# Kernel optimization log

Measured on AMD Instinct MI355X. Metric: run time of the kernel, lower is better.

## Reference

```python
import jax, jax.numpy as jnp
import numpy as np

N_PTS = 1 << 20          # query points
N_LEVELS = 8
BASE_RES, MAX_RES = 16, 512
GROWTH = (MAX_RES / BASE_RES) ** (1.0 / (N_LEVELS - 1))
RES = [int(np.floor(BASE_RES * GROWTH ** i)) for i in range(N_LEVELS)]
T = 1 << 19              # hash table size per level
F = 2                    # features per table entry
D = 64                   # per-level MLP width
NUM_OUT = 16
BOUND = 1.5

# 8 corner offsets of a unit cube, and NGP spatial-hash primes
OFFSETS = np.stack(np.meshgrid(*([[0, 1]] * 3), indexing='ij'), -1).reshape(8, 3)
PRIMES = np.array([1, 2654435761, 805459861], dtype=np.uint32)


def hash_interp(xn, table, res):
    """Trilinear hash-grid lookup. xn: [N,3] in [0,1), table: [T,F]."""
    pos = xn * res                                    # [N,3]
    p0f = jnp.floor(pos)
    w = pos - jax.lax.stop_gradient(p0f)              # [N,3] interp weights
    p0 = jax.lax.stop_gradient(p0f).astype(jnp.uint32)
    corners = p0[:, None, :] + jnp.asarray(OFFSETS.astype(np.uint32))[None]  # [N,8,3]
    hp = corners * jnp.asarray(PRIMES)[None, None, :]  # uint32 wraparound mul
    idx = (hp[..., 0] ^ hp[..., 1] ^ hp[..., 2]) & jnp.uint32(T - 1)  # [N,8]
    feats = table[idx]                                # [N,8,F] irregular gather
    off = jnp.asarray(OFFSETS.astype(np.float32))     # [8,3]
    wc = jnp.prod(off[None] * w[:, None, :] + (1.0 - off[None]) * (1.0 - w[:, None, :]), axis=-1)  # [N,8]
    return jnp.einsum('nc,ncf->nf', wc, feats)        # [N,F]


def fourier(h, B):
    """Fourier feature embed: h [N,D] @ B [N_freqs] -> [sin, cos]."""
    proj = (2.0 * jnp.pi) * (h @ B)                   # [N, D//2]
    return jnp.concatenate([jnp.sin(proj), jnp.cos(proj)], axis=-1)  # [N, D]


def setup_inputs() -> dict:
    key = jax.random.key(0)
    ks = jax.random.split(key, 12)
    inp = {
        'input': jax.random.normal(ks[0], (N_PTS, 3), jnp.float32),
        'W0': jax.random.normal(ks[1], (3, D), jnp.float32) * 0.3,
        'b0': jnp.zeros((D,), jnp.float32),
        'Ws': jax.random.normal(ks[2], (N_LEVELS - 1, D, D), jnp.float32) * (1.0 / np.sqrt(D)),
        'bs': jnp.zeros((N_LEVELS - 1, D), jnp.float32),
        'tables': jax.random.uniform(ks[3], (N_LEVELS, T, F), jnp.float32, -1e-2, 1e-2),
        'Gw': jax.random.normal(ks[4], (N_LEVELS, F, D), jnp.float32) * 0.5,
        'Gb': jnp.zeros((N_LEVELS, D), jnp.float32),
        'Bmat': jax.random.normal(ks[5], (N_LEVELS, D, D // 2), jnp.float32) * 0.25,
        'Wout': jax.random.normal(ks[6], (D, NUM_OUT), jnp.float32) * (1.0 / np.sqrt(D)),
        'bout': jnp.zeros((NUM_OUT,), jnp.float32),
    }
    return inp


def reference(input, W0, b0, Ws, bs, tables, Gw, Gb, Bmat, Wout, bout):
    x = input / BOUND                                  # [N,3]
    xn = jnp.clip((x + 1.0) * 0.5, 0.0, 1.0 - 1e-6)    # normalize to [0,1)
    h = x
    acc = jnp.zeros((input.shape[0], D), jnp.float32)
    for i in range(N_LEVELS):
        h = (h @ W0 + b0) if i == 0 else (h @ Ws[i - 1] + bs[i - 1])  # [N,D]
        g = hash_interp(xn, tables[i], float(RES[i]))  # [N,F] hash-grid feats
        hg = h + g @ Gw[i] + Gb[i]                     # fuse grid feats into channel
        acc = acc + fourier(hg, Bmat[i])               # [N,D] sin/cos embed, summed
    return acc @ Wout + bout                           # [N,NUM_OUT]
```

## Files before the change

### kernel.cpp

```cpp
#include <hip/hip_runtime.h>
#include <math.h>
#include <stdint.h>

#define N_LEVELS 8
#define TBITS 19
#define TMASK ((1u << TBITS) - 1u)
#define BLK 128

typedef __attribute__((ext_vector_type(8))) short short8;
typedef __attribute__((ext_vector_type(4))) float f32x4;
typedef unsigned int uint;
typedef unsigned short ushort;

#define WSW_OFF   0
#define WSW_N     (7 * 2 * 4 * 2 * 512)
#define WSB_OFF   (WSW_N * 2)
#define WSB_N     (8 * 2 * 2 * 2 * 512)
#define WSWO_OFF  (WSB_OFF + WSB_N * 2)
#define WSWO_N    (2 * 2 * 512)
#define WSP_OFF   (WSWO_OFF + WSWO_N * 2)
#define WSP_N     (8 * 3 * 32)
#define WS_NEEDED ((size_t)(WSP_OFF + WSP_N * 4))

struct ResArr { float r[N_LEVELS]; };

#define HIDX(pt, ch) ((((pt) << 6) | (ch)) ^ (((pt) & 7) << 3))

__device__ __forceinline__ ushort f2bf(float f) {
    uint u = __float_as_uint(f);
    u += 0x7fffu + ((u >> 16) & 1u);
    return (ushort)(u >> 16);
}
__device__ __forceinline__ float bf2f(ushort h) {
    return __uint_as_float(((uint)h) << 16);
}
__device__ __forceinline__ uint cvtpk(float a, float b) {
    uint r;
    asm("v_cvt_pk_bf16_f32 %0, %1, %2" : "=v"(r) : "v"(a), "v"(b));
    return r;
}
__device__ __forceinline__ short8 ldfragG(const void* p) {
    return __builtin_bit_cast(short8, *(const uint4*)p);
}
__device__ __forceinline__ short8 ldfragL(const ushort* p) {
    return __builtin_bit_cast(short8, *(const uint4*)p);
}
__device__ __forceinline__ f32x4 MFMA(short8 a, short8 b, f32x4 c) {
    return __builtin_amdgcn_mfma_f32_16x16x32_bf16(a, b, c, 0, 0, 0);
}
__device__ __forceinline__ f32x4 zero4() {
    f32x4 z; z[0] = 0.f; z[1] = 0.f; z[2] = 0.f; z[3] = 0.f; return z;
}
__device__ __forceinline__ float sin2pi(float t) {
    float f = t - floorf(t);
    return __builtin_amdgcn_sinf(f);
}
__device__ __forceinline__ float cos2pi(float t) {
    float f = t - floorf(t);
    return __builtin_amdgcn_cosf(f);
}

__global__ void prep_kernel(const float* __restrict__ Ws,
                            const float* __restrict__ Bmat,
                            const float* __restrict__ Wout,
                            const float* __restrict__ Gw,
                            const float* __restrict__ Gb,
                            void* __restrict__ ws)
{
    const int NW = WSW_N, NB = WSB_N, NWO = WSWO_N;
    const int NTOT = NW + NB + NWO + WSP_N;
    int t = blockIdx.x * 256 + threadIdx.x;
    if (t >= NTOT) return;
    ushort* w16 = (ushort*)ws;
    float* wsP = (float*)((char*)ws + WSP_OFF);

    if (t < NW) {
        int i = t & 7, lane = (t >> 3) & 63, ks = (t >> 9) & 1;
        int mb = (t >> 10) & 3, s = (t >> 12) & 1, lv = t >> 13;
        int gl = lane >> 4, il = lane & 15;
        int k = ks * 32 + gl * 8 + i, m = mb * 16 + il;
        float v = Ws[lv * 4096 + k * 64 + m];
        ushort hi = f2bf(v);
        w16[t] = s ? f2bf(v - bf2f(hi)) : hi;
    } else if (t < NW + NB) {
        int u = t - NW;
        int i = u & 7, lane = (u >> 3) & 63, ks = (u >> 9) & 1;
        int mb = (u >> 10) & 1, s = (u >> 11) & 1, lv = u >> 12;
        int gl = lane >> 4, il = lane & 15;
        int k = ks * 32 + gl * 8 + i, m = mb * 16 + il;
        float v = Bmat[lv * 2048 + k * 32 + m];
        ushort hi = f2bf(v);
        w16[NW + u] = s ? f2bf(v - bf2f(hi)) : hi;
    } else if (t < NW + NB + NWO) {
        int u = t - NW - NB;
        int i = u & 7, lane = (u >> 3) & 63, ks = (u >> 9) & 1, s = (u >> 10) & 1;
        int gl = lane >> 4, il = lane & 15;
        int k = ks * 32 + gl * 8 + i;
        float v = Wout[k * 16 + il];
        ushort hi = f2bf(v);
        w16[(WSWO_OFF / 2) + u] = s ? f2bf(v - bf2f(hi)) : hi;
    } else {
        int u = t - NW - NB - NWO;
        int lv = u / 96, rem = u % 96, wh = rem >> 5, m = rem & 31;
        const float* src = (wh == 0) ? (Gw + lv * 128)
                         : (wh == 1) ? (Gw + lv * 128 + 64)
                                     : (Gb + lv * 64);
        float acc = 0.f;
        for (int j = 0; j < 64; ++j)
            acc = fmaf(src[j], Bmat[lv * 2048 + j * 32 + m], acc);
        wsP[lv * 96 + wh * 32 + m] = acc;
    }
}

__global__ __launch_bounds__(64) void ffb_mfma(
    const float* __restrict__ input,
    const float* __restrict__ W0,
    const float* __restrict__ b0,
    const float* __restrict__ bs,
    const float* __restrict__ tables,
    const float* __restrict__ bout,
    const void* __restrict__ ws,
    float* __restrict__ out,
    int npts, ResArr ra)
{
    __shared__ __attribute__((aligned(16))) ushort sHhi[2048];
    __shared__ __attribute__((aligned(16))) ushort sHlo[2048];
    __shared__ __attribute__((aligned(16))) ushort sF[2048];
    __shared__ float sW0[256];
    __shared__ float sP[96];
    __shared__ float sBias[64];
    __shared__ float sG[64];
    __shared__ float sBout[16];

    const int l = threadIdx.x;
    const int il = l & 15, gl = l >> 4;
    const int base = blockIdx.x * 32;
    const int p = l & 31;
    const char* wsc = (const char*)ws;
    const float* wsP = (const float*)(wsc + WSP_OFF);

    float x0 = input[(size_t)(base + p) * 3 + 0] * (1.0f / 1.5f);
    float x1 = input[(size_t)(base + p) * 3 + 1] * (1.0f / 1.5f);
    float x2 = input[(size_t)(base + p) * 3 + 2] * (1.0f / 1.5f);
    const float hiclip = (float)(1.0 - 1e-6);
    float xn0 = fminf(fmaxf((x0 + 1.0f) * 0.5f, 0.0f), hiclip);
    float xn1 = fminf(fmaxf((x1 + 1.0f) * 0.5f, 0.0f), hiclip);
    float xn2 = fminf(fmaxf((x2 + 1.0f) * 0.5f, 0.0f), hiclip);

    short8 aWo[2];
#pragma unroll
    for (int ks = 0; ks < 2; ++ks)
        aWo[ks] = ldfragG(wsc + WSWO_OFF + (size_t)(0 * 2 + ks) * 1024 + l * 16);

    f32x4 outacc[2];
    outacc[0] = zero4(); outacc[1] = zero4();
    short8 bH[2][2][2];

    for (int lev = 0; lev < N_LEVELS; ++lev) {
        if (lev == 0) {
            for (int j = l; j < 192; j += 64) sW0[j] = W0[j];
            sW0[192 + l] = b0[l];
            if (l < 16) sBout[l] = bout[l];
        } else {
            sBias[l] = bs[(lev - 1) * 64 + l];
        }
        sP[l] = wsP[lev * 96 + l];
        if (l < 32) sP[64 + l] = wsP[lev * 96 + 64 + l];
        if (l < 32) {
            const float res = ra.r[lev];
            float px = xn0 * res, py = xn1 * res, pz = xn2 * res;
            float fx = floorf(px), fy = floorf(py), fz = floorf(pz);
            float wx = px - fx, wy = py - fy, wz = pz - fz;
            uint ix = (uint)fx, iy = (uint)fy, iz = (uint)fz;
            const float* __restrict__ tab = tables + (((size_t)lev) << TBITS) * 2;
            float g0 = 0.f, g1 = 0.f;
#pragma unroll
            for (int c = 0; c < 8; ++c) {
                const uint bx = (c >> 2) & 1, by = (c >> 1) & 1, bz = c & 1;
                uint hx = ix + bx;
                uint hy = (iy + by) * 2654435761u;
                uint hz = (iz + bz) * 805459861u;
                uint idx = (hx ^ hy ^ hz) & TMASK;
                float f0 = tab[(size_t)idx * 2 + 0];
                float f1 = tab[(size_t)idx * 2 + 1];
                float wc = (bx ? wx : 1.0f - wx) * (by ? wy : 1.0f - wy) * (bz ? wz : 1.0f - wz);
                g0 = fmaf(wc, f0, g0);
                g1 = fmaf(wc, f1, g1);
            }
            sG[2 * l] = g0; sG[2 * l + 1] = g1;
        }
        __syncthreads();

        if (lev == 0) {
            const int chb = (l >> 5) * 32;
#pragma unroll
            for (int cc = 0; cc < 32; cc += 2) {
                int ch = chb + cc;
                float v0 = fmaf(x0, sW0[ch],     fmaf(x1, sW0[64 + ch],     fmaf(x2, sW0[128 + ch],     sW0[192 + ch])));
                float v1 = fmaf(x0, sW0[ch + 1], fmaf(x1, sW0[64 + ch + 1], fmaf(x2, sW0[128 + ch + 1], sW0[192 + ch + 1])));
                uint pk = cvtpk(v0, v1);
                float r0 = v0 - __uint_as_float(pk << 16);
                float r1 = v1 - __uint_as_float(pk & 0xffff0000u);
                uint pklo = cvtpk(r0, r1);
                uint idx = HIDX(p, ch);
                *(uint*)&sHhi[idx] = pk;
                *(uint*)&sHlo[idx] = pklo;
            }
        } else {
            f32x4 acc[4][2];
#pragma unroll
            for (int mb = 0; mb < 4; ++mb)
#pragma unroll
                for (int nb = 0; nb < 2; ++nb) acc[mb][nb] = zero4();
#pragma unroll
            for (int mb = 0; mb < 4; ++mb) {
                short8 aHi[2], aLo[2];
#pragma unroll
                for (int ks = 0; ks < 2; ++ks) {
                    aHi[ks] = ldfragG(wsc + WSW_OFF + (size_t)((((lev - 1) * 2 + 0) * 4 + mb) * 2 + ks) * 1024 + l * 16);
                    aLo[ks] = ldfragG(wsc + WSW_OFF + (size_t)((((lev - 1) * 2 + 1) * 4 + mb) * 2 + ks) * 1024 + l * 16);
                }
#pragma unroll
                for (int nb = 0; nb < 2; ++nb)
#pragma unroll
                    for (int ks = 0; ks < 2; ++ks) {
                        acc[mb][nb] = MFMA(aHi[ks], bH[0][ks][nb], acc[mb][nb]);
                        acc[mb][nb] = MFMA(aLo[ks], bH[0][ks][nb], acc[mb][nb]);
                        acc[mb][nb] = MFMA(aHi[ks], bH[1][ks][nb], acc[mb][nb]);
                    }
            }
#pragma unroll
            for (int mb = 0; mb < 4; ++mb)
#pragma unroll
                for (int nb = 0; nb < 2; ++nb) {
                    int pt = nb * 16 + il, ch0 = mb * 16 + gl * 4;
                    float2 ba = *(float2*)&sBias[ch0];
                    float2 bb = *(float2*)&sBias[ch0 + 2];
                    float v0 = acc[mb][nb][0] + ba.x, v1 = acc[mb][nb][1] + ba.y;
                    float v2 = acc[mb][nb][2] + bb.x, v3 = acc[mb][nb][3] + bb.y;
                    uint pkA = cvtpk(v0, v1), pkB = cvtpk(v2, v3);
                    float r0 = v0 - __uint_as_float(pkA << 16);
                    float r1 = v1 - __uint_as_float(pkA & 0xffff0000u);
                    float r2 = v2 - __uint_as_float(pkB << 16);
                    float r3 = v3 - __uint_as_float(pkB & 0xffff0000u);
                    uint pkLA = cvtpk(r0, r1), pkLB = cvtpk(r2, r3);
                    uint idx = HIDX(pt, ch0);
                    *(uint*)&sHhi[idx] = pkA;  *(uint*)&sHhi[idx + 2] = pkB;
                    *(uint*)&sHlo[idx] = pkLA; *(uint*)&sHlo[idx + 2] = pkLB;
                }
        }
        __syncthreads();

#pragma unroll
        for (int ks = 0; ks < 2; ++ks)
#pragma unroll
            for (int nb = 0; nb < 2; ++nb) {
                int pt = nb * 16 + il;
                uint idx = HIDX(pt, ks * 32 + gl * 8);
                bH[0][ks][nb] = ldfragL(&sHhi[idx]);
                bH[1][ks][nb] = ldfragL(&sHlo[idx]);
            }

        f32x4 pacc[2][2];
#pragma unroll
        for (int mb = 0; mb < 2; ++mb)
#pragma unroll
            for (int nb = 0; nb < 2; ++nb) pacc[mb][nb] = zero4();
#pragma unroll
        for (int mb = 0; mb < 2; ++mb) {
            short8 aBhi[2], aBlo[2];
#pragma unroll
            for (int ks = 0; ks < 2; ++ks) {
                aBhi[ks] = ldfragG(wsc + WSB_OFF + (size_t)(((lev * 2 + 0) * 2 + mb) * 2 + ks) * 1024 + l * 16);
                aBlo[ks] = ldfragG(wsc + WSB_OFF + (size_t)(((lev * 2 + 1) * 2 + mb) * 2 + ks) * 1024 + l * 16);
            }
#pragma unroll
            for (int nb = 0; nb < 2; ++nb)
#pragma unroll
                for (int ks = 0; ks < 2; ++ks) {
                    pacc[mb][nb] = MFMA(aBhi[ks], bH[0][ks][nb], pacc[mb][nb]);
                    pacc[mb][nb] = MFMA(aBlo[ks], bH[0][ks][nb], pacc[mb][nb]);
                    pacc[mb][nb] = MFMA(aBhi[ks], bH[1][ks][nb], pacc[mb][nb]);
                }
        }

#pragma unroll
        for (int mb = 0; mb < 2; ++mb)
#pragma unroll
            for (int nb = 0; nb < 2; ++nb) {
                int pt = nb * 16 + il, m0 = mb * 16 + gl * 4;
                float2 g   = *(float2*)&sG[pt * 2];
                float2 p0a = *(float2*)&sP[m0],      p0b = *(float2*)&sP[m0 + 2];
                float2 p1a = *(float2*)&sP[32 + m0], p1b = *(float2*)&sP[32 + m0 + 2];
                float2 p2a = *(float2*)&sP[64 + m0], p2b = *(float2*)&sP[64 + m0 + 2];
                float t0 = pacc[mb][nb][0] + fmaf(g.x, p0a.x, fmaf(g.y, p1a.x, p2a.x));
                float t1 = pacc[mb][nb][1] + fmaf(g.x, p0a.y, fmaf(g.y, p1a.y, p2a.y));
                float t2 = pacc[mb][nb][2] + fmaf(g.x, p0b.x, fmaf(g.y, p1b.x, p2b.x));
                float t3 = pacc[mb][nb][3] + fmaf(g.x, p0b.y, fmaf(g.y, p1b.y, p2b.y));
                float s0 = sin2pi(t0), s1 = sin2pi(t1), s2 = sin2pi(t2), s3 = sin2pi(t3);
                float c0 = cos2pi(t0), c1 = cos2pi(t1), c2 = cos2pi(t2), c3 = cos2pi(t3);
                uint idxs = HIDX(pt, m0), idxc = HIDX(pt, 32 + m0);
                *(uint*)&sF[idxs]     = cvtpk(s0, s1);
                *(uint*)&sF[idxs + 2] = cvtpk(s2, s3);
                *(uint*)&sF[idxc]     = cvtpk(c0, c1);
                *(uint*)&sF[idxc + 2] = cvtpk(c2, c3);
            }
        __syncthreads();

#pragma unroll
        for (int nb = 0; nb < 2; ++nb)
#pragma unroll
            for (int ks = 0; ks < 2; ++ks) {
                int pt = nb * 16 + il;
                short8 bF = ldfragL(&sF[HIDX(pt, ks * 32 + gl * 8)]);
                outacc[nb] = MFMA(aWo[ks], bF, outacc[nb]);
            }
    }

#pragma unroll
    for (int nb = 0; nb < 2; ++nb) {
        int pt = nb * 16 + il;
        float4 v;
        v.x = outacc[nb][0] + sBout[gl * 4 + 0];
        v.y = outacc[nb][1] + sBout[gl * 4 + 1];
        v.z = outacc[nb][2] + sBout[gl * 4 + 2];
        v.w = outacc[nb][3] + sBout[gl * 4 + 3];
        *(float4*)(&out[(size_t)(base + pt) * 16 + gl * 4]) = v;
    }
}

__global__ __launch_bounds__(BLK) void ffb_valu(
    const float* __restrict__ input,
    const float* __restrict__ W0,
    const float* __restrict__ b0,
    const float* __restrict__ Ws,
    const float* __restrict__ bs,
    const float* __restrict__ tables,
    const float* __restrict__ Gw,
    const float* __restrict__ Gb,
    const float* __restrict__ Bmat,
    const float* __restrict__ Wout,
    const float* __restrict__ bout,
    float* __restrict__ out,
    int npts, ResArr resarr)
{
    __shared__ float lds_h[64][BLK];

    const int tid = threadIdx.x;
    const int n = blockIdx.x * BLK + tid;
    if (n >= npts) return;

    float x0 = input[(size_t)n * 3 + 0] / 1.5f;
    float x1 = input[(size_t)n * 3 + 1] / 1.5f;
    float x2 = input[(size_t)n * 3 + 2] / 1.5f;
    const float hi = (float)(1.0 - 1e-6);
    float xn0 = fminf(fmaxf((x0 + 1.0f) * 0.5f, 0.0f), hi);
    float xn1 = fminf(fmaxf((x1 + 1.0f) * 0.5f, 0.0f), hi);
    float xn2 = fminf(fmaxf((x2 + 1.0f) * 0.5f, 0.0f), hi);

    float outacc[16];
#pragma unroll
    for (int o = 0; o < 16; ++o) outacc[o] = 0.0f;

    for (int lev = 0; lev < N_LEVELS; ++lev) {
        float nh[64];
        if (lev == 0) {
#pragma unroll
            for (int j = 0; j < 64; ++j)
                nh[j] = fmaf(x0, W0[j], fmaf(x1, W0[64 + j], fmaf(x2, W0[128 + j], b0[j])));
        } else {
            const float* __restrict__ Wl = Ws + (size_t)(lev - 1) * 4096;
            const float* __restrict__ bl = bs + (size_t)(lev - 1) * 64;
#pragma unroll
            for (int j = 0; j < 64; ++j) nh[j] = bl[j];
            for (int k = 0; k < 64; ++k) {
                float hk = lds_h[k][tid];
                const float* __restrict__ wrow = Wl + (size_t)k * 64;
#pragma unroll
                for (int j = 0; j < 64; ++j)
                    nh[j] = fmaf(hk, wrow[j], nh[j]);
            }
        }
#pragma unroll
        for (int j = 0; j < 64; ++j) lds_h[j][tid] = nh[j];

        const float res = resarr.r[lev];
        float px = xn0 * res, py = xn1 * res, pz = xn2 * res;
        float fx = floorf(px), fy = floorf(py), fz = floorf(pz);
        float wx = px - fx, wy = py - fy, wz = pz - fz;
        uint32_t ix = (uint32_t)fx, iy = (uint32_t)fy, iz = (uint32_t)fz;
        const float* __restrict__ tab = tables + ((size_t)lev << TBITS) * 2;
        float g0 = 0.0f, g1 = 0.0f;
#pragma unroll
        for (int c = 0; c < 8; ++c) {
            const uint32_t bx = (c >> 2) & 1, by = (c >> 1) & 1, bz = c & 1;
            uint32_t hx = (ix + bx);
            uint32_t hy = (iy + by) * 2654435761u;
            uint32_t hz = (iz + bz) * 805459861u;
            uint32_t idx = (hx ^ hy ^ hz) & TMASK;
            float f0 = tab[(size_t)idx * 2 + 0];
            float f1 = tab[(size_t)idx * 2 + 1];
            float wc = (bx ? wx : 1.0f - wx) * (by ? wy : 1.0f - wy) * (bz ? wz : 1.0f - wz);
            g0 = fmaf(wc, f0, g0);
            g1 = fmaf(wc, f1, g1);
        }

        const float* __restrict__ Gw0 = Gw + (size_t)lev * 128;
        const float* __restrict__ Gw1 = Gw0 + 64;
        const float* __restrict__ Gbl = Gb + (size_t)lev * 64;
        const float* __restrict__ Bl  = Bmat + (size_t)lev * 2048;
        float proj[32];
#pragma unroll
        for (int m = 0; m < 32; ++m) proj[m] = 0.0f;
        for (int j = 0; j < 64; ++j) {
            float hgj = lds_h[j][tid] + fmaf(g0, Gw0[j], fmaf(g1, Gw1[j], Gbl[j]));
            const float* __restrict__ brow = Bl + (size_t)j * 32;
#pragma unroll
            for (int m = 0; m < 32; ++m)
                proj[m] = fmaf(hgj, brow[m], proj[m]);
        }

#pragma unroll
        for (int m = 0; m < 32; ++m) {
            float s = sin2pi(proj[m]);
            float c = cos2pi(proj[m]);
            const float* __restrict__ wsrow = Wout + (size_t)m * 16;
            const float* __restrict__ wcrow = Wout + (size_t)(m + 32) * 16;
#pragma unroll
            for (int o = 0; o < 16; ++o)
                outacc[o] = fmaf(s, wsrow[o], fmaf(c, wcrow[o], outacc[o]));
        }
    }

#pragma unroll
    for (int o = 0; o < 16; ++o)
        out[(size_t)n * 16 + o] = outacc[o] + bout[o];
}

extern "C" void kernel_launch(void* const* d_in, const int* in_sizes, int n_in,
                              void* d_out, int out_size, void* d_ws, size_t ws_size,
                              hipStream_t stream) {
    const float* input  = (const float*)d_in[0];
    const float* W0     = (const float*)d_in[1];
    const float* b0     = (const float*)d_in[2];
    const float* Ws     = (const float*)d_in[3];
    const float* bs     = (const float*)d_in[4];
    const float* tables = (const float*)d_in[5];
    const float* Gw     = (const float*)d_in[6];
    const float* Gb     = (const float*)d_in[7];
    const float* Bmat   = (const float*)d_in[8];
    const float* Wout   = (const float*)d_in[9];
    const float* bout   = (const float*)d_in[10];
    float* out = (float*)d_out;

    const int npts = in_sizes[0] / 3;

    ResArr ra;
    const double growth = pow(512.0 / 16.0, 1.0 / (double)(N_LEVELS - 1));
    for (int i = 0; i < N_LEVELS; ++i)
        ra.r[i] = (float)floor(16.0 * pow(growth, (double)i));

    if (ws_size >= WS_NEEDED && (npts % 32) == 0) {
        const int NTOT = WSW_N + WSB_N + WSWO_N + WSP_N;
        hipLaunchKernelGGL(prep_kernel, dim3((NTOT + 255) / 256), dim3(256), 0, stream,
                           Ws, Bmat, Wout, Gw, Gb, d_ws);
        hipLaunchKernelGGL(ffb_mfma, dim3(npts / 32), dim3(64), 0, stream,
                           input, W0, b0, bs, tables, bout, d_ws, out, npts, ra);
    } else {
        hipLaunchKernelGGL(ffb_valu, dim3((npts + BLK - 1) / BLK), dim3(BLK), 0, stream,
                           input, W0, b0, Ws, bs, tables, Gw, Gb, Bmat, Wout, bout,
                           out, npts, ra);
    }
}
```

Before: 765.0 us.

## Shrink shared memory by aliasing buffers and use fract intrinsic for sin/cos

Merges the hi/lo H buffers and the Fourier feature buffer into one 4096-entry shared array, with the F buffer reusing the lo region. It also drops the shared W0 and bout staging in favour of direct global reads. This cuts per-block LDS so more 64-thread blocks fit per CU, and launch bounds now ask for 4 waves per EU. sin/cos range reduction uses the hardware fract instruction instead of floor and subtract. Reusing the lo region relies on the barrier ordering between the bH loads and the F writes.

```diff
diff --git a/kernel.cpp b/kernel.cpp
--- a/kernel.cpp
+++ b/kernel.cpp
@@ -25,6 +25,7 @@
 struct ResArr { float r[N_LEVELS]; };
 
 #define HIDX(pt, ch) ((((pt) << 6) | (ch)) ^ (((pt) & 7) << 3))
+#define HLO 2048
 
 __device__ __forceinline__ ushort f2bf(float f) {
     uint u = __float_as_uint(f);
@@ -52,12 +53,10 @@
     f32x4 z; z[0] = 0.f; z[1] = 0.f; z[2] = 0.f; z[3] = 0.f; return z;
 }
 __device__ __forceinline__ float sin2pi(float t) {
-    float f = t - floorf(t);
-    return __builtin_amdgcn_sinf(f);
+    return __builtin_amdgcn_sinf(__builtin_amdgcn_fractf(t));
 }
 __device__ __forceinline__ float cos2pi(float t) {
-    float f = t - floorf(t);
-    return __builtin_amdgcn_cosf(f);
+    return __builtin_amdgcn_cosf(__builtin_amdgcn_fractf(t));
 }
 
 __global__ void prep_kernel(const float* __restrict__ Ws,
@@ -112,7 +111,7 @@
     }
 }
 
-__global__ __launch_bounds__(64) void ffb_mfma(
+__global__ __launch_bounds__(64, 4) void ffb_mfma(
     const float* __restrict__ input,
     const float* __restrict__ W0,
     const float* __restrict__ b0,
@@ -123,14 +122,10 @@
     float* __restrict__ out,
     int npts, ResArr ra)
 {
-    __shared__ __attribute__((aligned(16))) ushort sHhi[2048];
-    __shared__ __attribute__((aligned(16))) ushort sHlo[2048];
-    __shared__ __attribute__((aligned(16))) ushort sF[2048];
-    __shared__ float sW0[256];
+    __shared__ __attribute__((aligned(16))) ushort sH[4096];
     __shared__ float sP[96];
     __shared__ float sBias[64];
     __shared__ float sG[64];
-    __shared__ float sBout[16];
 
     const int l = threadIdx.x;
     const int il = l & 15, gl = l >> 4;
@@ -150,20 +145,14 @@
     short8 aWo[2];
 #pragma unroll
     for (int ks = 0; ks < 2; ++ks)
-        aWo[ks] = ldfragG(wsc + WSWO_OFF + (size_t)(0 * 2 + ks) * 1024 + l * 16);
+        aWo[ks] = ldfragG(wsc + WSWO_OFF + (size_t)ks * 1024 + l * 16);
 
     f32x4 outacc[2];
     outacc[0] = zero4(); outacc[1] = zero4();
     short8 bH[2][2][2];
 
     for (int lev = 0; lev < N_LEVELS; ++lev) {
-        if (lev == 0) {
-            for (int j = l; j < 192; j += 64) sW0[j] = W0[j];
-            sW0[192 + l] = b0[l];
-            if (l < 16) sBout[l] = bout[l];
-        } else {
-            sBias[l] = bs[(lev - 1) * 64 + l];
-        }
+        if (lev > 0) sBias[l] = bs[(lev - 1) * 64 + l];
         sP[l] = wsP[lev * 96 + l];
         if (l < 32) sP[64 + l] = wsP[lev * 96 + 64 + l];
         if (l < 32) {
@@ -196,15 +185,15 @@
 #pragma unroll
             for (int cc = 0; cc < 32; cc += 2) {
                 int ch = chb + cc;
-                float v0 = fmaf(x0, sW0[ch],     fmaf(x1, sW0[64 + ch],     fmaf(x2, sW0[128 + ch],     sW0[192 + ch])));
-                float v1 = fmaf(x0, sW0[ch + 1], fmaf(x1, sW0[64 + ch + 1], fmaf(x2, sW0[128 + ch + 1], sW0[192 + ch + 1])));
+                float v0 = fmaf(x0, W0[ch],     fmaf(x1, W0[64 + ch],     fmaf(x2, W0[128 + ch],     b0[ch])));
+                float v1 = fmaf(x0, W0[ch + 1], fmaf(x1, W0[64 + ch + 1], fmaf(x2, W0[128 + ch + 1], b0[ch + 1])));
                 uint pk = cvtpk(v0, v1);
                 float r0 = v0 - __uint_as_float(pk << 16);
                 float r1 = v1 - __uint_as_float(pk & 0xffff0000u);
                 uint pklo = cvtpk(r0, r1);
                 uint idx = HIDX(p, ch);
-                *(uint*)&sHhi[idx] = pk;
-                *(uint*)&sHlo[idx] = pklo;
+                *(uint*)&sH[idx] = pk;
+                *(uint*)&sH[HLO + idx] = pklo;
             }
         } else {
             f32x4 acc[4][2];
@@ -245,8 +234,8 @@
                     float r3 = v3 - __uint_as_float(pkB & 0xffff0000u);
                     uint pkLA = cvtpk(r0, r1), pkLB = cvtpk(r2, r3);
                     uint idx = HIDX(pt, ch0);
-                    *(uint*)&sHhi[idx] = pkA;  *(uint*)&sHhi[idx + 2] = pkB;
-                    *(uint*)&sHlo[idx] = pkLA; *(uint*)&sHlo[idx + 2] = pkLB;
+                    *(uint*)&sH[idx] = pkA;        *(uint*)&sH[idx + 2] = pkB;
+                    *(uint*)&sH[HLO + idx] = pkLA; *(uint*)&sH[HLO + idx + 2] = pkLB;
                 }
         }
         __syncthreads();
@@ -257,8 +246,8 @@
             for (int nb = 0; nb < 2; ++nb) {
                 int pt = nb * 16 + il;
                 uint idx = HIDX(pt, ks * 32 + gl * 8);
-                bH[0][ks][nb] = ldfragL(&sHhi[idx]);
-                bH[1][ks][nb] = ldfragL(&sHlo[idx]);
+                bH[0][ks][nb] = ldfragL(&sH[idx]);
+                bH[1][ks][nb] = ldfragL(&sH[HLO + idx]);
             }
 
         f32x4 pacc[2][2];
@@ -300,10 +289,10 @@
                 float s0 = sin2pi(t0), s1 = sin2pi(t1), s2 = sin2pi(t2), s3 = sin2pi(t3);
                 float c0 = cos2pi(t0), c1 = cos2pi(t1), c2 = cos2pi(t2), c3 = cos2pi(t3);
                 uint idxs = HIDX(pt, m0), idxc = HIDX(pt, 32 + m0);
-                *(uint*)&sF[idxs]     = cvtpk(s0, s1);
-                *(uint*)&sF[idxs + 2] = cvtpk(s2, s3);
-                *(uint*)&sF[idxc]     = cvtpk(c0, c1);
-                *(uint*)&sF[idxc + 2] = cvtpk(c2, c3);
+                *(uint*)&sH[HLO + idxs]     = cvtpk(s0, s1);
+                *(uint*)&sH[HLO + idxs + 2] = cvtpk(s2, s3);
+                *(uint*)&sH[HLO + idxc]     = cvtpk(c0, c1);
+                *(uint*)&sH[HLO + idxc + 2] = cvtpk(c2, c3);
             }
         __syncthreads();
 
@@ -312,7 +301,7 @@
 #pragma unroll
             for (int ks = 0; ks < 2; ++ks) {
                 int pt = nb * 16 + il;
-                short8 bF = ldfragL(&sF[HIDX(pt, ks * 32 + gl * 8)]);
+                short8 bF = ldfragL(&sH[HLO + HIDX(pt, ks * 32 + gl * 8)]);
                 outacc[nb] = MFMA(aWo[ks], bF, outacc[nb]);
             }
     }
@@ -321,10 +310,10 @@
     for (int nb = 0; nb < 2; ++nb) {
         int pt = nb * 16 + il;
         float4 v;
-        v.x = outacc[nb][0] + sBout[gl * 4 + 0];
-        v.y = outacc[nb][1] + sBout[gl * 4 + 1];
-        v.z = outacc[nb][2] + sBout[gl * 4 + 2];
-        v.w = outacc[nb][3] + sBout[gl * 4 + 3];
+        v.x = outacc[nb][0] + bout[gl * 4 + 0];
+        v.y = outacc[nb][1] + bout[gl * 4 + 1];
+        v.z = outacc[nb][2] + bout[gl * 4 + 2];
+        v.w = outacc[nb][3] + bout[gl * 4 + 3];
         *(float4*)(&out[(size_t)(base + pt) * 16 + gl * 4]) = v;
     }
 }
```

Measured after the change: 691.4 us. -9.6%, faster.
